# Optimization experiments

Hardware: AMD Instinct MI355X
Metric: run time of the kernel (lower is better)

## Reference

```python
import jax, jax.numpy as jnp
import numpy as np

B, S, E, H = 4, 2048, 1024, 16
HD = E // H  # head_dim = 64
EPS = 1.1920928955078125e-07  # torch.finfo(float32).eps (RMSNorm eps=None default)


def _rmsnorm(x, w):
    # normalize over last dim
    ms = jnp.mean(x * x, axis=-1, keepdims=True)
    return x * jax.lax.rsqrt(ms + EPS) * w


def _rope(x, start_pos=0):
    # x: [B, H, S, HD]; interleaved (even/odd) rotary embedding
    seq_len = x.shape[-2]
    inv_freq = 1.0 / (10000.0 ** (jnp.arange(0, HD, 2, dtype=jnp.float32) / HD))  # [HD/2]
    t = jnp.arange(start_pos, start_pos + seq_len, dtype=jnp.float32)  # [S]
    freqs = t[:, None] * inv_freq[None, :]  # [S, HD/2]
    cos = jnp.cos(freqs)[None, None]  # [1,1,S,HD/2]
    sin = jnp.sin(freqs)[None, None]
    x1 = x[..., 0::2]
    x2 = x[..., 1::2]
    o1 = x1 * cos - x2 * sin
    o2 = x1 * sin + x2 * cos
    # stack(..., -1).flatten(-2) -> re-interleave
    return jnp.stack((o1, o2), axis=-1).reshape(x.shape)


def setup_inputs() -> dict:
    key = jax.random.key(0)
    k1, k2, k3, k4 = jax.random.split(key, 4)
    lim = 1.0 / np.sqrt(E)
    return {
        "q": jax.random.normal(k1, (B, S, E), jnp.float32),
        "k": jax.random.normal(k2, (B, S, E), jnp.float32),
        "v": jax.random.normal(k3, (B, S, E), jnp.float32),
        "q_norm_w": jnp.ones((HD,), jnp.float32),
        "k_norm_w": jnp.ones((HD,), jnp.float32),
        "proj_w": jax.random.uniform(k4, (E, E), jnp.float32, -lim, lim),
        "proj_b": jnp.zeros((E,), jnp.float32),
    }


def reference(q, k, v, q_norm_w, k_norm_w, proj_w, proj_b):
    b, s, _ = q.shape
    scale = HD ** -0.5
    # [B,S,E] -> [B,H,S,HD]
    qh = q.reshape(b, s, H, HD).transpose(0, 2, 1, 3)
    kh = k.reshape(b, s, H, HD).transpose(0, 2, 1, 3)
    vh = v.reshape(b, s, H, HD).transpose(0, 2, 1, 3)
    # per-head QK RMSNorm then RoPE
    qh = _rope(_rmsnorm(qh, q_norm_w))
    kh = _rope(_rmsnorm(kh, k_norm_w))
    # explicit attention (no mask path)
    scores = jnp.einsum("bhqd,bhkd->bhqk", qh, kh) * scale  # [B,H,S,S]
    attn = jax.nn.softmax(scores, axis=-1)
    ctx = jnp.einsum("bhqk,bhkd->bhqd", attn, vh)
    ctx = ctx.transpose(0, 2, 1, 3).reshape(b, s, E)
    return ctx @ proj_w.T + proj_b
```

## Files before the change

### kernel.cpp

```cpp
#include <hip/hip_runtime.h>
#include <hip/hip_bf16.h>
#include <cstdint>

#define B_ 4
#define S_ 2048
#define E_ 1024
#define H_ 16
#define HD_ 64
#define EPS_ 1.1920928955078125e-07f

typedef __attribute__((ext_vector_type(8))) short shortx8;
typedef __attribute__((ext_vector_type(4))) float floatx4;
typedef __attribute__((ext_vector_type(4))) _Float16 halfx4;
typedef __attribute__((ext_vector_type(8))) _Float16 halfx8;

#define C1_ 0.18033688068389154f

__global__ __launch_bounds__(256) void prep(
    const float* __restrict__ q, const float* __restrict__ k,
    const float* __restrict__ v,
    const float* __restrict__ qw, const float* __restrict__ kw,
    const float* __restrict__ pw,
    __hip_bfloat16* __restrict__ qh, __hip_bfloat16* __restrict__ kh,
    _Float16* __restrict__ vt, __hip_bfloat16* __restrict__ wb)
{
    __shared__ _Float16 tile[64][72];
    const int bid = blockIdx.x;
    const int tid = threadIdx.x;

    if (bid < 16384) {
        const size_t PT = (size_t)B_ * S_ * E_ / 4;
        size_t t = (size_t)bid * 256 + tid;
        const bool is_k = (t >= PT);
        if (is_k) t -= PT;

        const int row = (int)(t >> 8);
        const int b   = row / S_;
        const int s   = row % S_;
        const int grp = (int)(t & 255);
        const int h   = grp >> 4;
        const int dl  = (grp & 15) * 4;

        const float* __restrict__ src = is_k ? k : q;
        const float* __restrict__ w   = is_k ? kw : qw;
        __hip_bfloat16* __restrict__ dst = is_k ? kh : qh;

        const float4 x  = ((const float4*)src)[t];
        const float4 wv = ((const float4*)w)[grp & 15];

        float ss = x.x * x.x + x.y * x.y + x.z * x.z + x.w * x.w;
#pragma unroll
        for (int m = 1; m < 16; m <<= 1) ss += __shfl_xor(ss, m);
        float r = rsqrtf(ss * (1.0f / HD_) + EPS_);
        if (!is_k) r *= C1_;

        const float xn0 = x.x * r * wv.x;
        const float xn1 = x.y * r * wv.y;
        const float xn2 = x.z * r * wv.z;
        const float xn3 = x.w * r * wv.w;

        const float L2I = 0.41524101186092029f;
        const int   i0  = dl >> 1;
        const float f0  = (float)s * exp2f(-(float)i0 * L2I);
        const float f1  = (float)s * exp2f(-(float)(i0 + 1) * L2I);
        const float c0 = __cosf(f0), sn0 = __sinf(f0);
        const float c1 = __cosf(f1), sn1 = __sinf(f1);

        __hip_bfloat16 pk[4];
        pk[0] = __float2bfloat16(xn0 * c0 - xn1 * sn0);
        pk[1] = __float2bfloat16(xn0 * sn0 + xn1 * c0);
        pk[2] = __float2bfloat16(xn2 * c1 - xn3 * sn1);
        pk[3] = __float2bfloat16(xn2 * sn1 + xn3 * c1);
        *(ushort4*)(dst + ((size_t)((b * H_ + h) * S_ + s)) * HD_ + dl) =
            *(const ushort4*)pk;
    } else if (bid < 18432) {
        const int bb2 = bid - 16384;
        const int s0  = (bb2 & 31) * 64;
        const int bh  = bb2 >> 5;
        const int b   = bh >> 4, h = bh & 15;
        {
            const int sl = tid >> 2;
            const int d0 = (tid & 3) * 16;
            const float* __restrict__ src =
                v + ((size_t)(b * S_ + s0 + sl)) * E_ + h * HD_ + d0;
            float4 f0 = ((const float4*)src)[0];
            float4 f1 = ((const float4*)src)[1];
            float4 f2 = ((const float4*)src)[2];
            float4 f3 = ((const float4*)src)[3];
            float vals[16] = {f0.x,f0.y,f0.z,f0.w, f1.x,f1.y,f1.z,f1.w,
                              f2.x,f2.y,f2.z,f2.w, f3.x,f3.y,f3.z,f3.w};
#pragma unroll
            for (int j = 0; j < 16; ++j)
                tile[d0 + j][sl] = (_Float16)vals[j];
        }
        __syncthreads();
        {
            const int d  = tid >> 2;
            const int sg = (tid & 3) * 16;
            _Float16* __restrict__ dst =
                vt + ((size_t)(bh * HD_ + d)) * S_ + s0 + sg;
            ((uint4*)dst)[0] = *(const uint4*)&tile[d][sg];
            ((uint4*)dst)[1] = *(const uint4*)&tile[d][sg + 8];
        }
    } else {
        const int i = (bid - 18432) * 256 + tid;
        float4 f = ((const float4*)pw)[i];
        wb[4 * i + 0] = __float2bfloat16(f.x);
        wb[4 * i + 1] = __float2bfloat16(f.y);
        wb[4 * i + 2] = __float2bfloat16(f.z);
        wb[4 * i + 3] = __float2bfloat16(f.w);
    }
}

__global__ __launch_bounds__(256, 4) void attn(
    const __hip_bfloat16* __restrict__ qh, const __hip_bfloat16* __restrict__ kh,
    const _Float16* __restrict__ vt, __hip_bfloat16* __restrict__ ctx)
{
    __shared__ __hip_bfloat16 Kt[128][72];
    __shared__ _Float16       Vt[64][152];

    const int bid  = blockIdx.x;
    const int slot = bid >> 3;
    const int bh   = ((bid & 7) << 3) | (slot & 7);
    const int q0   = (slot >> 3) * 128;
    const int tid  = threadIdx.x;
    const int wv   = tid >> 6;
    const int lane = tid & 63;
    const int l16  = lane & 15;
    const int quad = lane >> 4;
    const int b    = bh >> 4, h = bh & 15;

    shortx8 aq[2][2];
#pragma unroll
    for (int mh = 0; mh < 2; ++mh) {
        const __hip_bfloat16* qbase =
            qh + ((size_t)bh * S_ + q0 + wv * 32 + mh * 16 + l16) * HD_;
        aq[mh][0] = *(const shortx8*)(qbase + quad * 8);
        aq[mh][1] = *(const shortx8*)(qbase + 32 + quad * 8);
    }

    const halfx8 ones = {(_Float16)1.f, (_Float16)1.f, (_Float16)1.f, (_Float16)1.f,
                         (_Float16)1.f, (_Float16)1.f, (_Float16)1.f, (_Float16)1.f};

    floatx4 O[2][4] = {};
    floatx4 O5[2]   = {};

    const __hip_bfloat16* __restrict__ kbase = kh + (size_t)bh * S_ * HD_;
    const _Float16* __restrict__ vbase = vt + (size_t)bh * HD_ * S_;

    const int sr = tid >> 1, sc = (tid & 1) * 32;
    const int vr = tid >> 2, vc = (tid & 3) * 32;

    for (int kt = 0; kt < S_ / 128; ++kt) {
        {
            const __hip_bfloat16* kp = kbase + ((size_t)(kt * 128 + sr)) * HD_ + sc;
            uint4 k0 = ((const uint4*)kp)[0];
            uint4 k1 = ((const uint4*)kp)[1];
            uint4 k2 = ((const uint4*)kp)[2];
            uint4 k3 = ((const uint4*)kp)[3];
            *(uint4*)&Kt[sr][sc]      = k0;
            *(uint4*)&Kt[sr][sc + 8]  = k1;
            *(uint4*)&Kt[sr][sc + 16] = k2;
            *(uint4*)&Kt[sr][sc + 24] = k3;
            const _Float16* vp = vbase + (size_t)vr * S_ + kt * 128 + vc;
            uint4 v0 = ((const uint4*)vp)[0];
            uint4 v1 = ((const uint4*)vp)[1];
            uint4 v2 = ((const uint4*)vp)[2];
            uint4 v3 = ((const uint4*)vp)[3];
            *(uint4*)&Vt[vr][vc]      = v0;
            *(uint4*)&Vt[vr][vc + 8]  = v1;
            *(uint4*)&Vt[vr][vc + 16] = v2;
            *(uint4*)&Vt[vr][vc + 24] = v3;
        }
        __syncthreads();

#pragma unroll
        for (int hk = 0; hk < 2; ++hk) {
            floatx4 s4[2][4];
#pragma unroll
            for (int nt = 0; nt < 4; ++nt) {
                const shortx8 kb0 =
                    *(const shortx8*)&Kt[hk * 64 + nt * 16 + l16][quad * 8];
                const shortx8 kb1 =
                    *(const shortx8*)&Kt[hk * 64 + nt * 16 + l16][32 + quad * 8];
#pragma unroll
                for (int mh = 0; mh < 2; ++mh) {
                    floatx4 c = {0.f, 0.f, 0.f, 0.f};
                    c = __builtin_amdgcn_mfma_f32_16x16x32_bf16(kb0, aq[mh][0], c, 0, 0, 0);
                    c = __builtin_amdgcn_mfma_f32_16x16x32_bf16(kb1, aq[mh][1], c, 0, 0, 0);
                    s4[mh][nt] = c;
                }
            }

            halfx8 bb[2][2];
#pragma unroll
            for (int mh = 0; mh < 2; ++mh)
#pragma unroll
                for (int f = 0; f < 2; ++f) {
                    halfx8 hb;
#pragma unroll
                    for (int r = 0; r < 4; ++r)
                        hb[r] = (_Float16)exp2f(s4[mh][2 * f][r]);
#pragma unroll
                    for (int r = 0; r < 4; ++r)
                        hb[4 + r] = (_Float16)exp2f(s4[mh][2 * f + 1][r]);
                    bb[mh][f] = hb;
                }

#pragma unroll
            for (int mh = 0; mh < 2; ++mh) {
                O5[mh] = __builtin_amdgcn_mfma_f32_16x16x32_f16(ones, bb[mh][0], O5[mh], 0, 0, 0);
                O5[mh] = __builtin_amdgcn_mfma_f32_16x16x32_f16(ones, bb[mh][1], O5[mh], 0, 0, 0);
            }

#pragma unroll
            for (int dt = 0; dt < 4; ++dt) {
                const _Float16* vrow = &Vt[dt * 16 + l16][hk * 64];
                const halfx4 a0 = *(const halfx4*)(vrow + quad * 4);
                const halfx4 a1 = *(const halfx4*)(vrow + 16 + quad * 4);
                const halfx4 a2 = *(const halfx4*)(vrow + 32 + quad * 4);
                const halfx4 a3 = *(const halfx4*)(vrow + 48 + quad * 4);
                const halfx8 A0 = __builtin_shufflevector(a0, a1, 0, 1, 2, 3, 4, 5, 6, 7);
                const halfx8 A1 = __builtin_shufflevector(a2, a3, 0, 1, 2, 3, 4, 5, 6, 7);
#pragma unroll
                for (int mh = 0; mh < 2; ++mh) {
                    O[mh][dt] = __builtin_amdgcn_mfma_f32_16x16x32_f16(
                        A0, bb[mh][0], O[mh][dt], 0, 0, 0);
                    O[mh][dt] = __builtin_amdgcn_mfma_f32_16x16x32_f16(
                        A1, bb[mh][1], O[mh][dt], 0, 0, 0);
                }
            }
        }
        __syncthreads();
    }

#pragma unroll
    for (int mh = 0; mh < 2; ++mh) {
        const float inv = 1.0f / O5[mh][0];
        const int s = q0 + wv * 32 + mh * 16 + l16;
        __hip_bfloat16* cb = ctx + ((size_t)(b * S_ + s)) * E_ + h * HD_;
#pragma unroll
        for (int dt = 0; dt < 4; ++dt) {
            __hip_bfloat16 pk[4];
#pragma unroll
            for (int r = 0; r < 4; ++r)
                pk[r] = __float2bfloat16(O[mh][dt][r] * inv);
            *(ushort4*)(cb + dt * 16 + quad * 4) = *(const ushort4*)pk;
        }
    }
}

__global__ __launch_bounds__(256) void proj(
    const __hip_bfloat16* __restrict__ ctx, const __hip_bfloat16* __restrict__ wb,
    const float* __restrict__ bias, float* __restrict__ out)
{
    __shared__ __hip_bfloat16 As[128][40];
    __shared__ __hip_bfloat16 Bs[128][40];

    const int bid  = blockIdx.x;
    const int slot = bid >> 3;
    const int mblk = ((bid & 7) << 3) | (slot & 7);
    const int nblk = slot >> 3;
    const int m0 = mblk * 128;
    const int n0 = nblk * 128;
    const int tid  = threadIdx.x;
    const int wv   = tid >> 6;
    const int lane = tid & 63;
    const int l16  = lane & 15;
    const int quad = lane >> 4;
    const int wr   = (wv >> 1) * 64;
    const int wc   = (wv & 1) * 64;

    const int srow = tid >> 1;
    const int scol = (tid & 1) * 16;

    floatx4 acc[4][4] = {};

    for (int k0 = 0; k0 < E_; k0 += 32) {
        const uint4* ap = (const uint4*)(ctx + (size_t)(m0 + srow) * E_ + k0 + scol);
        const uint4* bp = (const uint4*)(wb  + (size_t)(n0 + srow) * E_ + k0 + scol);
        uint4 a0 = ap[0], a1 = ap[1];
        uint4 b0 = bp[0], b1 = bp[1];
        *(uint4*)&As[srow][scol]     = a0;
        *(uint4*)&As[srow][scol + 8] = a1;
        *(uint4*)&Bs[srow][scol]     = b0;
        *(uint4*)&Bs[srow][scol + 8] = b1;
        __syncthreads();

        shortx8 af[4], bf[4];
#pragma unroll
        for (int mt = 0; mt < 4; ++mt)
            af[mt] = *(const shortx8*)&As[wr + mt * 16 + l16][quad * 8];
#pragma unroll
        for (int nt = 0; nt < 4; ++nt)
            bf[nt] = *(const shortx8*)&Bs[wc + nt * 16 + l16][quad * 8];

#pragma unroll
        for (int mt = 0; mt < 4; ++mt)
#pragma unroll
            for (int nt = 0; nt < 4; ++nt)
                acc[mt][nt] = __builtin_amdgcn_mfma_f32_16x16x32_bf16(
                    af[mt], bf[nt], acc[mt][nt], 0, 0, 0);
        __syncthreads();
    }

#pragma unroll
    for (int nt = 0; nt < 4; ++nt) {
        const float bv = bias[n0 + wc + nt * 16 + l16];
#pragma unroll
        for (int mt = 0; mt < 4; ++mt)
#pragma unroll
            for (int r = 0; r < 4; ++r) {
                const int mrow = m0 + wr + mt * 16 + quad * 4 + r;
                const int ncol = n0 + wc + nt * 16 + l16;
                out[(size_t)mrow * E_ + ncol] = acc[mt][nt][r] + bv;
            }
    }
}

extern "C" void kernel_launch(void* const* d_in, const int* in_sizes, int n_in,
                              void* d_out, int out_size, void* d_ws, size_t ws_size,
                              hipStream_t stream)
{
    const float* q  = (const float*)d_in[0];
    const float* k  = (const float*)d_in[1];
    const float* v  = (const float*)d_in[2];
    const float* qw = (const float*)d_in[3];
    const float* kw = (const float*)d_in[4];
    const float* pw = (const float*)d_in[5];
    const float* pb = (const float*)d_in[6];
    float* out = (float*)d_out;

    char* ws = (char*)d_ws;
    const size_t SEG = (size_t)B_ * H_ * S_ * HD_ * 2;
    __hip_bfloat16* qh  = (__hip_bfloat16*)(ws);
    __hip_bfloat16* kh  = (__hip_bfloat16*)(ws + SEG);
    _Float16*       vt  = (_Float16*)(ws + 2 * SEG);
    __hip_bfloat16* ctx = (__hip_bfloat16*)(ws + 3 * SEG);
    __hip_bfloat16* wbp = (__hip_bfloat16*)(ws + 4 * SEG);

    prep<<<dim3(19456), 256, 0, stream>>>(q, k, v, qw, kw, pw, qh, kh, vt, wbp);
    attn<<<dim3(1024), 256, 0, stream>>>(qh, kh, vt, ctx);
    proj<<<dim3(512), 256, 0, stream>>>(ctx, wbp, pb, out);
}
```

Before: 279.9 us.

## Permute V^T layout for 16-byte LDS reads, use fast exp/pack, deepen proj K-tile

The V transpose in prep now writes each 64-element row in a permuted order, so the attention kernel can load each MFMA A operand with a single 8-half LDS read instead of two 4-half reads plus a shuffle. The softmax exponentials use the hardware exp2 intrinsic and packed round-toward-zero f16 conversion. The projection GEMM doubles its K tile to 64, halving the number of barriers per output tile at the cost of more LDS per block. These changes trade some rounding behaviour (RTZ, approximate exp2) for fewer instructions.

```diff
diff --git a/kernel.cpp b/kernel.cpp
--- a/kernel.cpp
+++ b/kernel.cpp
@@ -13,6 +13,7 @@
 typedef __attribute__((ext_vector_type(4))) float floatx4;
 typedef __attribute__((ext_vector_type(4))) _Float16 halfx4;
 typedef __attribute__((ext_vector_type(8))) _Float16 halfx8;
+typedef __attribute__((ext_vector_type(2))) __fp16 fp16x2;
 
 #define C1_ 0.18033688068389154f
 
@@ -61,8 +62,8 @@
 
         const float L2I = 0.41524101186092029f;
         const int   i0  = dl >> 1;
-        const float f0  = (float)s * exp2f(-(float)i0 * L2I);
-        const float f1  = (float)s * exp2f(-(float)(i0 + 1) * L2I);
+        const float f0  = (float)s * __builtin_amdgcn_exp2f(-(float)i0 * L2I);
+        const float f1  = (float)s * __builtin_amdgcn_exp2f(-(float)(i0 + 1) * L2I);
         const float c0 = __cosf(f0), sn0 = __sinf(f0);
         const float c1 = __cosf(f1), sn1 = __sinf(f1);
 
@@ -97,10 +98,14 @@
         {
             const int d  = tid >> 2;
             const int sg = (tid & 3) * 16;
-            _Float16* __restrict__ dst =
-                vt + ((size_t)(bh * HD_ + d)) * S_ + s0 + sg;
-            ((uint4*)dst)[0] = *(const uint4*)&tile[d][sg];
-            ((uint4*)dst)[1] = *(const uint4*)&tile[d][sg + 8];
+            _Float16* __restrict__ dstrow =
+                vt + ((size_t)(bh * HD_ + d)) * S_ + s0;
+#pragma unroll
+            for (int g = 0; g < 4; ++g) {
+                const int o = sg + 4 * g;
+                const int n = (o & 32) + (((o & 15) >> 2) << 3) + (((o >> 4) & 1) << 2);
+                *(ushort4*)(dstrow + n) = *(const ushort4*)&tile[d][o];
+            }
         }
     } else {
         const int i = (bid - 18432) * 256 + tid;
@@ -197,14 +202,20 @@
             for (int mh = 0; mh < 2; ++mh)
 #pragma unroll
                 for (int f = 0; f < 2; ++f) {
-                    halfx8 hb;
-#pragma unroll
-                    for (int r = 0; r < 4; ++r)
-                        hb[r] = (_Float16)exp2f(s4[mh][2 * f][r]);
-#pragma unroll
-                    for (int r = 0; r < 4; ++r)
-                        hb[4 + r] = (_Float16)exp2f(s4[mh][2 * f + 1][r]);
-                    bb[mh][f] = hb;
+                    union { fp16x2 h2[4]; halfx8 h8; } u;
+                    u.h2[0] = __builtin_amdgcn_cvt_pkrtz(
+                        __builtin_amdgcn_exp2f(s4[mh][2 * f][0]),
+                        __builtin_amdgcn_exp2f(s4[mh][2 * f][1]));
+                    u.h2[1] = __builtin_amdgcn_cvt_pkrtz(
+                        __builtin_amdgcn_exp2f(s4[mh][2 * f][2]),
+                        __builtin_amdgcn_exp2f(s4[mh][2 * f][3]));
+                    u.h2[2] = __builtin_amdgcn_cvt_pkrtz(
+                        __builtin_amdgcn_exp2f(s4[mh][2 * f + 1][0]),
+                        __builtin_amdgcn_exp2f(s4[mh][2 * f + 1][1]));
+                    u.h2[3] = __builtin_amdgcn_cvt_pkrtz(
+                        __builtin_amdgcn_exp2f(s4[mh][2 * f + 1][2]),
+                        __builtin_amdgcn_exp2f(s4[mh][2 * f + 1][3]));
+                    bb[mh][f] = u.h8;
                 }
 
 #pragma unroll
@@ -216,12 +227,8 @@
 #pragma unroll
             for (int dt = 0; dt < 4; ++dt) {
                 const _Float16* vrow = &Vt[dt * 16 + l16][hk * 64];
-                const halfx4 a0 = *(const halfx4*)(vrow + quad * 4);
-                const halfx4 a1 = *(const halfx4*)(vrow + 16 + quad * 4);
-                const halfx4 a2 = *(const halfx4*)(vrow + 32 + quad * 4);
-                const halfx4 a3 = *(const halfx4*)(vrow + 48 + quad * 4);
-                const halfx8 A0 = __builtin_shufflevector(a0, a1, 0, 1, 2, 3, 4, 5, 6, 7);
-                const halfx8 A1 = __builtin_shufflevector(a2, a3, 0, 1, 2, 3, 4, 5, 6, 7);
+                const halfx8 A0 = *(const halfx8*)(vrow + quad * 8);
+                const halfx8 A1 = *(const halfx8*)(vrow + 32 + quad * 8);
 #pragma unroll
                 for (int mh = 0; mh < 2; ++mh) {
                     O[mh][dt] = __builtin_amdgcn_mfma_f32_16x16x32_f16(
@@ -254,8 +261,8 @@
     const __hip_bfloat16* __restrict__ ctx, const __hip_bfloat16* __restrict__ wb,
     const float* __restrict__ bias, float* __restrict__ out)
 {
-    __shared__ __hip_bfloat16 As[128][40];
-    __shared__ __hip_bfloat16 Bs[128][40];
+    __shared__ __hip_bfloat16 As[128][72];
+    __shared__ __hip_bfloat16 Bs[128][72];
 
     const int bid  = blockIdx.x;
     const int slot = bid >> 3;
@@ -272,35 +279,42 @@
     const int wc   = (wv & 1) * 64;
 
     const int srow = tid >> 1;
-    const int scol = (tid & 1) * 16;
+    const int scol = (tid & 1) * 32;
 
     floatx4 acc[4][4] = {};
 
-    for (int k0 = 0; k0 < E_; k0 += 32) {
+    for (int k0 = 0; k0 < E_; k0 += 64) {
         const uint4* ap = (const uint4*)(ctx + (size_t)(m0 + srow) * E_ + k0 + scol);
         const uint4* bp = (const uint4*)(wb  + (size_t)(n0 + srow) * E_ + k0 + scol);
-        uint4 a0 = ap[0], a1 = ap[1];
-        uint4 b0 = bp[0], b1 = bp[1];
-        *(uint4*)&As[srow][scol]     = a0;
-        *(uint4*)&As[srow][scol + 8] = a1;
-        *(uint4*)&Bs[srow][scol]     = b0;
-        *(uint4*)&Bs[srow][scol + 8] = b1;
-        __syncthreads();
-
-        shortx8 af[4], bf[4];
-#pragma unroll
-        for (int mt = 0; mt < 4; ++mt)
-            af[mt] = *(const shortx8*)&As[wr + mt * 16 + l16][quad * 8];
-#pragma unroll
-        for (int nt = 0; nt < 4; ++nt)
-            bf[nt] = *(const shortx8*)&Bs[wc + nt * 16 + l16][quad * 8];
-
-#pragma unroll
-        for (int mt = 0; mt < 4; ++mt)
+        uint4 a0 = ap[0], a1 = ap[1], a2 = ap[2], a3 = ap[3];
+        uint4 b0 = bp[0], b1 = bp[1], b2 = bp[2], b3 = bp[3];
+        *(uint4*)&As[srow][scol]      = a0;
+        *(uint4*)&As[srow][scol + 8]  = a1;
+        *(uint4*)&As[srow][scol + 16] = a2;
+        *(uint4*)&As[srow][scol + 24] = a3;
+        *(uint4*)&Bs[srow][scol]      = b0;
+        *(uint4*)&Bs[srow][scol + 8]  = b1;
+        *(uint4*)&Bs[srow][scol + 16] = b2;
+        *(uint4*)&Bs[srow][scol + 24] = b3;
+        __syncthreads();
+
+#pragma unroll
+        for (int ks = 0; ks < 2; ++ks) {
+            shortx8 af[4], bf[4];
+#pragma unroll
+            for (int mt = 0; mt < 4; ++mt)
+                af[mt] = *(const shortx8*)&As[wr + mt * 16 + l16][ks * 32 + quad * 8];
 #pragma unroll
             for (int nt = 0; nt < 4; ++nt)
-                acc[mt][nt] = __builtin_amdgcn_mfma_f32_16x16x32_bf16(
-                    af[mt], bf[nt], acc[mt][nt], 0, 0, 0);
+                bf[nt] = *(const shortx8*)&Bs[wc + nt * 16 + l16][ks * 32 + quad * 8];
+
+#pragma unroll
+            for (int mt = 0; mt < 4; ++mt)
+#pragma unroll
+                for (int nt = 0; nt < 4; ++nt)
+                    acc[mt][nt] = __builtin_amdgcn_mfma_f32_16x16x32_bf16(
+                        af[mt], bf[nt], acc[mt][nt], 0, 0, 0);
+        }
         __syncthreads();
     }
 
```

After: 252.8 us. 1.11x faster.
